# Kernel tuning notes

Measured on AMD Instinct MI355X. Metric: run time of the kernel, lower is better.

Reference implementation:

```python
import jax, jax.numpy as jnp
import numpy as np

B, L, H, V = 16, 128, 1024, 50257

def setup_inputs() -> dict:
    key = jax.random.key(0)
    ks = jax.random.split(key, 12)
    s_h = 1.0 / np.sqrt(H)
    s_l = 1.0 / np.sqrt(L)
    return {
        "input": jax.random.randint(ks[0], (B, L), 0, V, dtype=jnp.int64) if jax.config.jax_enable_x64 else jax.random.randint(ks[0], (B, L), 0, V, dtype=jnp.int32),
        "hidden": jax.random.normal(ks[1], (B, L, H), dtype=jnp.float32),
        "emb": jax.random.normal(ks[2], (V, H), dtype=jnp.float32),
        "bridge_w": jax.random.uniform(ks[3], (1, L), jnp.float32, -s_l, s_l),
        "bridge_b": jax.random.uniform(ks[4], (1,), jnp.float32, -s_l, s_l),
        "w_ih": jax.random.uniform(ks[5], (3 * H, H), jnp.float32, -s_h, s_h),
        "w_hh": jax.random.uniform(ks[6], (3 * H, H), jnp.float32, -s_h, s_h),
        "b_ih": jax.random.uniform(ks[7], (3 * H,), jnp.float32, -s_h, s_h),
        "b_hh": jax.random.uniform(ks[8], (3 * H,), jnp.float32, -s_h, s_h),
        "proj_w": jax.random.uniform(ks[9], (V, H), jnp.float32, -s_h, s_h),
        "proj_b": jax.random.uniform(ks[10], (V,), jnp.float32, -s_h, s_h),
    }

def reference(input, hidden, emb, bridge_w, bridge_b, w_ih, w_hh, b_ih, b_hh, proj_w, proj_b):
    # step() only ever uses gru_output[0], which depends only on input[:,0] and
    # the bridged h0, so all (maxlen-1) teacher-forced steps are identical.
    x0 = jax.nn.relu(emb[input[:, 0]])                      # [B,H] embed + relu
    # bridge: hidden.transpose(1,2) [B,H,L] @ W[1,L]^T -> [B,H,1] -> h0 [B,H]
    h0 = jnp.einsum("blh,l->bh", hidden, bridge_w[0]) + bridge_b[0]
    # single GRU cell step (torch gate ordering r,z,n)
    gi = x0 @ w_ih.T + b_ih                                 # [B,3H]
    gh = h0 @ w_hh.T + b_hh                                 # [B,3H]
    ir, iz, in_ = jnp.split(gi, 3, axis=1)
    hr, hz, hn = jnp.split(gh, 3, axis=1)
    r = jax.nn.sigmoid(ir + hr)
    z = jax.nn.sigmoid(iz + hz)
    n = jnp.tanh(in_ + r * hn)
    h1 = (1.0 - z) * n + z * h0                             # [B,H]
    logp = jax.nn.log_softmax(h1 @ proj_w.T + proj_b, axis=1)  # [B,V]
    # stack of (maxlen-1) identical predictions
    return jnp.broadcast_to(logp[:, None, :], (logp.shape[0], L - 1, logp.shape[1]))
```

## Files before the change

kernel.cpp:

```cpp
#include <hip/hip_runtime.h>
#include <math.h>

#define BB 16
#define LL 128
#define HH 1024
#define VV 50257
#define VP 50260
#define NBLOG 786

__global__ __launch_bounds__(256) void k_embed_bridge(
    const int* __restrict__ input, const float* __restrict__ hidden,
    const float* __restrict__ emb, const float* __restrict__ bw,
    const float* __restrict__ bb, float* __restrict__ x0, float* __restrict__ h0) {
    int tid = blockIdx.x * 256 + threadIdx.x;
    int b = tid >> 10;
    int h = tid & (HH - 1);
    int tok = input[b * LL];
    float xv = emb[(long)tok * HH + h];
    x0[tid] = xv > 0.f ? xv : 0.f;
    float acc = bb[0];
    const float* hp = hidden + (long)b * LL * HH + h;
    #pragma unroll 8
    for (int l = 0; l < LL; ++l) acc += hp[(long)l * HH] * bw[l];
    h0[tid] = acc;
}

struct Smem {
    float  Wl[2][64 * 68];
    float4 hc[2][16 * 17];
    float  pb[64];
    float  redm[4][16];
    float  reds[4][16];
};

__device__ __forceinline__ void mv64_core(
    const float* __restrict__ W, int v0, int rowclamp,
    const float* __restrict__ vec, Smem& sm, float (&acc)[16][4]) {
    const int t    = threadIdx.x;
    const int lane = t & 63;
    const int w    = t >> 6;
    const int ks   = lane & 15;
    const int q4   = lane >> 4;
    const int srow = t >> 2, sq = t & 3;
    const int hb   = t >> 4, hq = t & 15;

    long grow = v0 + srow; if (grow > rowclamp) grow = rowclamp;
    const float* gW = W + grow * HH + sq * 4;
    const float* gH = vec + hb * HH + hq * 4;

    float4 w0, w1, w2, w3, hstg;
    {
        const float4* p = (const float4*)gW;
        w0 = p[0]; w1 = p[4]; w2 = p[8]; w3 = p[12];
        hstg = *(const float4*)gH;
    }
    #pragma unroll
    for (int r = 0; r < 16; ++r)
        acc[r][0] = acc[r][1] = acc[r][2] = acc[r][3] = 0.f;

    for (int c = 0; c < 16; ++c) {
        const int cur = c & 1;
        float*  WL = sm.Wl[cur];
        float4* HC = sm.hc[cur];
        float4* wr4 = (float4*)(WL + srow * 68);
        wr4[sq]      = w0;
        wr4[sq + 4]  = w1;
        wr4[sq + 8]  = w2;
        wr4[sq + 12] = w3;
        HC[hq * 17 + hb] = hstg;
        if (c < 15) {
            const float4* p = (const float4*)(gW + (c + 1) * 64);
            w0 = p[0]; w1 = p[4]; w2 = p[8]; w3 = p[12];
            hstg = *(const float4*)(gH + (c + 1) * 64);
        }
        __syncthreads();
        float4 h0v = HC[ks * 17 + q4 * 4 + 0];
        float4 h1v = HC[ks * 17 + q4 * 4 + 1];
        float4 h2v = HC[ks * 17 + q4 * 4 + 2];
        float4 h3v = HC[ks * 17 + q4 * 4 + 3];
        const float* wr = WL + (w * 16) * 68 + ks * 4;
        #pragma unroll
        for (int r = 0; r < 16; ++r) {
            float4 wv = *(const float4*)(wr + r * 68);
            acc[r][0] += wv.x * h0v.x + wv.y * h0v.y + wv.z * h0v.z + wv.w * h0v.w;
            acc[r][1] += wv.x * h1v.x + wv.y * h1v.y + wv.z * h1v.z + wv.w * h1v.w;
            acc[r][2] += wv.x * h2v.x + wv.y * h2v.y + wv.z * h2v.z + wv.w * h2v.w;
            acc[r][3] += wv.x * h3v.x + wv.y * h3v.y + wv.z * h3v.z + wv.w * h3v.w;
        }
    }
    #pragma unroll
    for (int m = 1; m <= 8; m <<= 1) {
        #pragma unroll
        for (int r = 0; r < 16; ++r) {
            acc[r][0] += __shfl_xor(acc[r][0], m, 64);
            acc[r][1] += __shfl_xor(acc[r][1], m, 64);
            acc[r][2] += __shfl_xor(acc[r][2], m, 64);
            acc[r][3] += __shfl_xor(acc[r][3], m, 64);
        }
    }
}

__global__ __launch_bounds__(256) void k_gates(
    const float* __restrict__ x0, const float* __restrict__ h0,
    const float* __restrict__ w_ih, const float* __restrict__ w_hh,
    const float* __restrict__ b_ih, const float* __restrict__ b_hh,
    float* __restrict__ gi_t, float* __restrict__ gh_t) {
    __shared__ Smem sm;
    const int blk = blockIdx.x;
    const bool second = blk >= 48;
    const float* W    = second ? w_hh : w_ih;
    const float* vec  = second ? h0 : x0;
    const float* bias = second ? b_hh : b_ih;
    float* outp       = second ? gh_t : gi_t;
    const int g0 = (second ? blk - 48 : blk) * 64;
    const int t = threadIdx.x;
    if (t < 64) sm.pb[t] = bias[g0 + t];

    float acc[16][4];
    mv64_core(W, g0, 3 * HH - 1, vec, sm, acc);

    const int lane = t & 63, w = t >> 6, ks = lane & 15, q4 = lane >> 4;
    #pragma unroll
    for (int r = 0; r < 16; ++r) {
        if (ks == r) {
            float bs = sm.pb[w * 16 + r];
            float4 o = make_float4(acc[r][0] + bs, acc[r][1] + bs,
                                   acc[r][2] + bs, acc[r][3] + bs);
            *(float4*)(outp + (g0 + w * 16 + r) * 16 + q4 * 4) = o;
        }
    }
}

__global__ __launch_bounds__(256) void k_combine(
    const float* __restrict__ gi_t, const float* __restrict__ gh_t,
    const float* __restrict__ h0, float* __restrict__ h1) {
    int tid = blockIdx.x * 256 + threadIdx.x;
    int h = tid >> 4;
    int b = tid & 15;
    float ir = gi_t[h * 16 + b],             hr = gh_t[h * 16 + b];
    float iz = gi_t[(HH + h) * 16 + b],      hz = gh_t[(HH + h) * 16 + b];
    float in_ = gi_t[(2 * HH + h) * 16 + b], hn = gh_t[(2 * HH + h) * 16 + b];
    float r = 1.f / (1.f + expf(-(ir + hr)));
    float z = 1.f / (1.f + expf(-(iz + hz)));
    float n = tanhf(in_ + r * hn);
    float h0v = h0[b * HH + h];
    h1[b * HH + h] = (1.f - z) * n + z * h0v;
}

__global__ __launch_bounds__(256) void k_logits_lse(
    const float* __restrict__ h1, const float* __restrict__ proj_w,
    const float* __restrict__ proj_b, float* __restrict__ logits,
    float* __restrict__ pmax, float* __restrict__ psum) {
    __shared__ Smem sm;
    const int t = threadIdx.x;
    const int v0 = blockIdx.x * 64;
    if (t < 64) {
        int gv = v0 + t;
        sm.pb[t] = (gv < VV) ? proj_b[gv] : -1e30f;
    }
    float acc[16][4];
    mv64_core(proj_w, v0, VV - 1, h1, sm, acc);

    const int lane = t & 63, w = t >> 6, ks = lane & 15, q4 = lane >> 4;
    float mx[4] = {-1e30f, -1e30f, -1e30f, -1e30f};
    #pragma unroll
    for (int r = 0; r < 16; ++r) {
        float pb = sm.pb[w * 16 + r];
        acc[r][0] += pb; acc[r][1] += pb; acc[r][2] += pb; acc[r][3] += pb;
        mx[0] = fmaxf(mx[0], acc[r][0]); mx[1] = fmaxf(mx[1], acc[r][1]);
        mx[2] = fmaxf(mx[2], acc[r][2]); mx[3] = fmaxf(mx[3], acc[r][3]);
    }
    float sv[4] = {0.f, 0.f, 0.f, 0.f};
    #pragma unroll
    for (int r = 0; r < 16; ++r) {
        sv[0] += __expf(acc[r][0] - mx[0]); sv[1] += __expf(acc[r][1] - mx[1]);
        sv[2] += __expf(acc[r][2] - mx[2]); sv[3] += __expf(acc[r][3] - mx[3]);
    }
    #pragma unroll
    for (int r = 0; r < 16; ++r) {
        if (ks == r) {
            int v = v0 + w * 16 + r;
            if (v < VV) {
                logits[(long)(q4 * 4 + 0) * VP + v] = acc[r][0];
                logits[(long)(q4 * 4 + 1) * VP + v] = acc[r][1];
                logits[(long)(q4 * 4 + 2) * VP + v] = acc[r][2];
                logits[(long)(q4 * 4 + 3) * VP + v] = acc[r][3];
            }
        }
    }
    if (ks == 0) {
        #pragma unroll
        for (int i = 0; i < 4; ++i) {
            sm.redm[w][q4 * 4 + i] = mx[i];
            sm.reds[w][q4 * 4 + i] = sv[i];
        }
    }
    __syncthreads();
    if (t < 16) {
        float M = sm.redm[0][t];
        M = fmaxf(M, sm.redm[1][t]); M = fmaxf(M, sm.redm[2][t]); M = fmaxf(M, sm.redm[3][t]);
        float S = sm.reds[0][t] * __expf(sm.redm[0][t] - M)
                + sm.reds[1][t] * __expf(sm.redm[1][t] - M)
                + sm.reds[2][t] * __expf(sm.redm[2][t] - M)
                + sm.reds[3][t] * __expf(sm.redm[3][t] - M);
        pmax[blockIdx.x * 16 + t] = M;
        psum[blockIdx.x * 16 + t] = S;
    }
}

__global__ __launch_bounds__(64) void k_lse_red(
    const float* __restrict__ pmax, const float* __restrict__ psum,
    float* __restrict__ C) {
    const int b = blockIdx.x;
    const int t = threadIdx.x;
    float M = -1e30f;
    for (int i = t; i < NBLOG; i += 64) M = fmaxf(M, pmax[i * 16 + b]);
    #pragma unroll
    for (int m = 32; m >= 1; m >>= 1) M = fmaxf(M, __shfl_xor(M, m, 64));
    float S = 0.f;
    for (int i = t; i < NBLOG; i += 64)
        S += psum[i * 16 + b] * __expf(pmax[i * 16 + b] - M);
    #pragma unroll
    for (int m = 32; m >= 1; m >>= 1) S += __shfl_xor(S, m, 64);
    if (t == 0) C[b] = M + logf(S);
}

__global__ __launch_bounds__(256) void k_bcast(
    const float* __restrict__ logits, const float* __restrict__ C,
    float* __restrict__ out) {
    const int b = blockIdx.y;
    const int t = threadIdx.x;
    const int v0 = blockIdx.x * 1024 + t;
    const float cb = C[b];
    const float* src = logits + (long)b * VP;
    const bool g0 = v0 < VV, g1 = v0 + 256 < VV, g2 = v0 + 512 < VV, g3 = v0 + 768 < VV;
    const float f0 = g0 ? src[v0]       - cb : 0.f;
    const float f1 = g1 ? src[v0 + 256] - cb : 0.f;
    const float f2 = g2 ? src[v0 + 512] - cb : 0.f;
    const float f3 = g3 ? src[v0 + 768] - cb : 0.f;
    long base = (long)b * 127 * VV + v0;
    for (int r = 0; r < 127; ++r) {
        float* d = out + base;
        if (g0) d[0]   = f0;
        if (g1) d[256] = f1;
        if (g2) d[512] = f2;
        if (g3) d[768] = f3;
        base += VV;
    }
}

extern "C" void kernel_launch(void* const* d_in, const int* in_sizes, int n_in,
                              void* d_out, int out_size, void* d_ws, size_t ws_size,
                              hipStream_t stream) {
    const int*   input    = (const int*)  d_in[0];
    const float* hidden   = (const float*)d_in[1];
    const float* emb      = (const float*)d_in[2];
    const float* bridge_w = (const float*)d_in[3];
    const float* bridge_b = (const float*)d_in[4];
    const float* w_ih     = (const float*)d_in[5];
    const float* w_hh     = (const float*)d_in[6];
    const float* b_ih     = (const float*)d_in[7];
    const float* b_hh     = (const float*)d_in[8];
    const float* proj_w   = (const float*)d_in[9];
    const float* proj_b   = (const float*)d_in[10];
    float* out = (float*)d_out;

    float* ws    = (float*)d_ws;
    float* x0    = ws;
    float* h0v   = ws + 16384;
    float* h1v   = ws + 32768;
    float* Cb    = ws + 49152;
    float* pmaxb = ws + 49168;
    float* psumb = ws + 61744;
    float* gi_t  = ws + 74320;
    float* gh_t  = ws + 123472;
    float* logits = ws + 74320;

    k_embed_bridge<<<dim3(64), dim3(256), 0, stream>>>(input, hidden, emb,
                                                       bridge_w, bridge_b, x0, h0v);
    k_gates<<<dim3(96), dim3(256), 0, stream>>>(x0, h0v, w_ih, w_hh, b_ih, b_hh,
                                                gi_t, gh_t);
    k_combine<<<dim3(64), dim3(256), 0, stream>>>(gi_t, gh_t, h0v, h1v);
    k_logits_lse<<<dim3(NBLOG), dim3(256), 0, stream>>>(h1v, proj_w, proj_b,
                                                        logits, pmaxb, psumb);
    k_lse_red<<<dim3(16), dim3(64), 0, stream>>>(pmaxb, psumb, Cb);
    k_bcast<<<dim3(50, 16), dim3(256), 0, stream>>>(logits, Cb, out);
}
```

Baseline: 755.7 us.

## Deepen matvec prefetch to two chunks, add occupancy hints, nontemporal broadcast stores

```diff
diff --git a/kernel.cpp b/kernel.cpp
--- a/kernel.cpp
+++ b/kernel.cpp
@@ -48,44 +48,78 @@
     const float* gW = W + grow * HH + sq * 4;
     const float* gH = vec + hb * HH + hq * 4;
 
-    float4 w0, w1, w2, w3, hstg;
+    float4 a0, a1, a2, a3, ahv;
+    float4 b0, b1, b2, b3, bhv;
     {
         const float4* p = (const float4*)gW;
-        w0 = p[0]; w1 = p[4]; w2 = p[8]; w3 = p[12];
-        hstg = *(const float4*)gH;
+        a0 = p[0]; a1 = p[4]; a2 = p[8]; a3 = p[12];
+        ahv = *(const float4*)gH;
+        const float4* q = (const float4*)(gW + 64);
+        b0 = q[0]; b1 = q[4]; b2 = q[8]; b3 = q[12];
+        bhv = *(const float4*)(gH + 64);
     }
     #pragma unroll
     for (int r = 0; r < 16; ++r)
         acc[r][0] = acc[r][1] = acc[r][2] = acc[r][3] = 0.f;
 
-    for (int c = 0; c < 16; ++c) {
-        const int cur = c & 1;
-        float*  WL = sm.Wl[cur];
-        float4* HC = sm.hc[cur];
-        float4* wr4 = (float4*)(WL + srow * 68);
-        wr4[sq]      = w0;
-        wr4[sq + 4]  = w1;
-        wr4[sq + 8]  = w2;
-        wr4[sq + 12] = w3;
-        HC[hq * 17 + hb] = hstg;
-        if (c < 15) {
-            const float4* p = (const float4*)(gW + (c + 1) * 64);
-            w0 = p[0]; w1 = p[4]; w2 = p[8]; w3 = p[12];
-            hstg = *(const float4*)(gH + (c + 1) * 64);
-        }
-        __syncthreads();
-        float4 h0v = HC[ks * 17 + q4 * 4 + 0];
-        float4 h1v = HC[ks * 17 + q4 * 4 + 1];
-        float4 h2v = HC[ks * 17 + q4 * 4 + 2];
-        float4 h3v = HC[ks * 17 + q4 * 4 + 3];
-        const float* wr = WL + (w * 16) * 68 + ks * 4;
-        #pragma unroll
-        for (int r = 0; r < 16; ++r) {
-            float4 wv = *(const float4*)(wr + r * 68);
-            acc[r][0] += wv.x * h0v.x + wv.y * h0v.y + wv.z * h0v.z + wv.w * h0v.w;
-            acc[r][1] += wv.x * h1v.x + wv.y * h1v.y + wv.z * h1v.z + wv.w * h1v.w;
-            acc[r][2] += wv.x * h2v.x + wv.y * h2v.y + wv.z * h2v.z + wv.w * h2v.w;
-            acc[r][3] += wv.x * h3v.x + wv.y * h3v.y + wv.z * h3v.z + wv.w * h3v.w;
+    for (int c = 0; c < 16; c += 2) {
+        {
+            float*  WL = sm.Wl[0];
+            float4* HC = sm.hc[0];
+            float4* wr4 = (float4*)(WL + srow * 68);
+            wr4[sq]      = a0;
+            wr4[sq + 4]  = a1;
+            wr4[sq + 8]  = a2;
+            wr4[sq + 12] = a3;
+            HC[hq * 17 + hb] = ahv;
+            if (c + 2 < 16) {
+                const float4* p = (const float4*)(gW + (c + 2) * 64);
+                a0 = p[0]; a1 = p[4]; a2 = p[8]; a3 = p[12];
+                ahv = *(const float4*)(gH + (c + 2) * 64);
+            }
+            __syncthreads();
+            float4 h0v = HC[ks * 17 + q4 * 4 + 0];
+            float4 h1v = HC[ks * 17 + q4 * 4 + 1];
+            float4 h2v = HC[ks * 17 + q4 * 4 + 2];
+            float4 h3v = HC[ks * 17 + q4 * 4 + 3];
+            const float* wr = WL + (w * 16) * 68 + ks * 4;
+            #pragma unroll
+            for (int r = 0; r < 16; ++r) {
+                float4 wv = *(const float4*)(wr + r * 68);
+                acc[r][0] += wv.x * h0v.x + wv.y * h0v.y + wv.z * h0v.z + wv.w * h0v.w;
+                acc[r][1] += wv.x * h1v.x + wv.y * h1v.y + wv.z * h1v.z + wv.w * h1v.w;
+                acc[r][2] += wv.x * h2v.x + wv.y * h2v.y + wv.z * h2v.z + wv.w * h2v.w;
+                acc[r][3] += wv.x * h3v.x + wv.y * h3v.y + wv.z * h3v.z + wv.w * h3v.w;
+            }
+        }
+        {
+            float*  WL = sm.Wl[1];
+            float4* HC = sm.hc[1];
+            float4* wr4 = (float4*)(WL + srow * 68);
+            wr4[sq]      = b0;
+            wr4[sq + 4]  = b1;
+            wr4[sq + 8]  = b2;
+            wr4[sq + 12] = b3;
+            HC[hq * 17 + hb] = bhv;
+            if (c + 3 < 16) {
+                const float4* p = (const float4*)(gW + (c + 3) * 64);
+                b0 = p[0]; b1 = p[4]; b2 = p[8]; b3 = p[12];
+                bhv = *(const float4*)(gH + (c + 3) * 64);
+            }
+            __syncthreads();
+            float4 h0v = HC[ks * 17 + q4 * 4 + 0];
+            float4 h1v = HC[ks * 17 + q4 * 4 + 1];
+            float4 h2v = HC[ks * 17 + q4 * 4 + 2];
+            float4 h3v = HC[ks * 17 + q4 * 4 + 3];
+            const float* wr = WL + (w * 16) * 68 + ks * 4;
+            #pragma unroll
+            for (int r = 0; r < 16; ++r) {
+                float4 wv = *(const float4*)(wr + r * 68);
+                acc[r][0] += wv.x * h0v.x + wv.y * h0v.y + wv.z * h0v.z + wv.w * h0v.w;
+                acc[r][1] += wv.x * h1v.x + wv.y * h1v.y + wv.z * h1v.z + wv.w * h1v.w;
+                acc[r][2] += wv.x * h2v.x + wv.y * h2v.y + wv.z * h2v.z + wv.w * h2v.w;
+                acc[r][3] += wv.x * h3v.x + wv.y * h3v.y + wv.z * h3v.z + wv.w * h3v.w;
+            }
         }
     }
     #pragma unroll
@@ -100,7 +134,7 @@
     }
 }
 
-__global__ __launch_bounds__(256) void k_gates(
+__global__ __launch_bounds__(256, 3) void k_gates(
     const float* __restrict__ x0, const float* __restrict__ h0,
     const float* __restrict__ w_ih, const float* __restrict__ w_hh,
     const float* __restrict__ b_ih, const float* __restrict__ b_hh,
@@ -147,7 +181,7 @@
     h1[b * HH + h] = (1.f - z) * n + z * h0v;
 }
 
-__global__ __launch_bounds__(256) void k_logits_lse(
+__global__ __launch_bounds__(256, 3) void k_logits_lse(
     const float* __restrict__ h1, const float* __restrict__ proj_w,
     const float* __restrict__ proj_b, float* __restrict__ logits,
     float* __restrict__ pmax, float* __restrict__ psum) {
@@ -241,10 +275,10 @@
     long base = (long)b * 127 * VV + v0;
     for (int r = 0; r < 127; ++r) {
         float* d = out + base;
-        if (g0) d[0]   = f0;
-        if (g1) d[256] = f1;
-        if (g2) d[512] = f2;
-        if (g3) d[768] = f3;
+        if (g0) __builtin_nontemporal_store(f0, d);
+        if (g1) __builtin_nontemporal_store(f1, d + 256);
+        if (g2) __builtin_nontemporal_store(f2, d + 512);
+        if (g3) __builtin_nontemporal_store(f3, d + 768);
         base += VV;
     }
 }
```

After: 975.7 us. +29.1%, slower.
